# Kernel optimization log

Hardware: AMD Instinct MI355X
Metric: run time of the kernel (lower is better)

The kernel has to match this reference:

```python
import jax, jax.numpy as jnp
import numpy as np

N, D = 1024, 256  # number of matrices (power of 2), matrix dim
EPS = 0.002       # near-identity noise scale to keep 1024-long product stable


def setup_inputs() -> dict:
    key = jax.random.key(0)
    k1, k2 = jax.random.split(key)
    x = jax.random.normal(k1, (1, D), dtype=jnp.float32)
    m = jnp.eye(D, dtype=jnp.float32)[None] + EPS * jax.random.normal(
        k2, (N, D, D), dtype=jnp.float32)
    return {"x": x, "m": m}


def reference(x, m):
    # The torch module performs a Blelloch up-sweep (pairwise bmm) building
    # per-level products, then a down-sweep producing the exclusive prefix
    # applications of x: res[k] = x @ (m_0 @ ... @ m_{k-1}) for k = 0..N.
    # lax.associative_scan with matmul is the idiomatic log-depth tree scan
    # computing the same math: P[k] = m_0 @ ... @ m_k (inclusive, in order).
    P = jax.lax.associative_scan(jnp.matmul, m)      # [N, D, D]
    applied = jnp.matmul(x, P)[:, 0, :]              # [N, D]: x @ P[k]
    # res[0] = x (empty prefix), res[1..N] = x @ P[0..N-1]
    res = jnp.concatenate([x, applied], axis=0)      # [N+1, D]
    return res
```

## Files before the change

kernel.cpp:

```cpp
#include <hip/hip_runtime.h>
#include <hip/hip_bf16.h>


#define D 256
#define DD 65536

typedef __attribute__((ext_vector_type(8))) short short8;
typedef __attribute__((ext_vector_type(4))) float f4;

__device__ __forceinline__ float bf2f(unsigned short u) {
  return __uint_as_float(((unsigned)u) << 16);
}
__device__ __forceinline__ unsigned short f2bf(float f) {
  __hip_bfloat16 h = __float2bfloat16(f);
  unsigned short u;
  __builtin_memcpy(&u, &h, 2);
  return u;
}
__device__ __forceinline__ unsigned f2bf2(float lo, float hi) {
  __hip_bfloat162 h = __float22bfloat162_rn(make_float2(lo, hi));
  unsigned u;
  __builtin_memcpy(&u, &h, 4);
  return u;
}
#define LSWZ(i15, lq) (((((i15) & 15)) + ((lq) << 4)) ^ (lq))

__global__ __launch_bounds__(256, 4) void gemm_mfma(
    const float* __restrict__ aF, const unsigned short* __restrict__ aBf,
    long aMul, long aOff,
    const float* __restrict__ bF, const unsigned short* __restrict__ bBf,
    long bMul, long bOff,
    unsigned short* __restrict__ out)
{
  __shared__ __attribute__((aligned(16))) unsigned short Bs[16384];

  const int  bx  = blockIdx.x;
  const int  nmb = ((int)gridDim.x) >> 4;
  const int  xcd = bx & 7, q = bx >> 3;
  const long mat = (long)(xcd * (nmb >> 3)) + (q >> 4);
  const int  tile = q & 15;
  const int  m0 = (tile >> 2) << 6, n0 = (tile & 3) << 6;
  const long aBase = (mat * aMul + aOff) * (long)DD;
  const long bBase = (mat * bMul + bOff) * (long)DD;
  const int t = threadIdx.x;
  const int w = t >> 6, l = t & 63, lm = l & 15, lq4 = l >> 4;
  const int lswz = l ^ lq4;

  const int R = m0 + (w << 4) + lm;
  short8 areg[8];
  if (aF) {
    const float* ap = aF + aBase + (long)R * D + (lq4 << 3);
#pragma unroll
    for (int kt = 0; kt < 8; ++kt) {
      float4 v0 = *(const float4*)(ap + (kt << 5));
      float4 v1 = *(const float4*)(ap + (kt << 5) + 4);
      if ((R >> 3) == (kt << 2) + lq4) {
        const int j = R & 7;
        if      (j == 0) v0.x -= 1.f;
        else if (j == 1) v0.y -= 1.f;
        else if (j == 2) v0.z -= 1.f;
        else if (j == 3) v0.w -= 1.f;
        else if (j == 4) v1.x -= 1.f;
        else if (j == 5) v1.y -= 1.f;
        else if (j == 6) v1.z -= 1.f;
        else             v1.w -= 1.f;
      }
      union { short8 v8; unsigned u[4]; } ou;
      ou.u[0] = f2bf2(v0.x, v0.y);
      ou.u[1] = f2bf2(v0.z, v0.w);
      ou.u[2] = f2bf2(v1.x, v1.y);
      ou.u[3] = f2bf2(v1.z, v1.w);
      areg[kt] = ou.v8;
    }
  } else {
    const unsigned short* ap = aBf + aBase + (long)R * D + (lq4 << 3);
#pragma unroll
    for (int kt = 0; kt < 8; ++kt)
      areg[kt] = *(const short8*)(ap + (kt << 5));
  }

  {
    const int n4 = (t & 15) << 2;
    const int kb0 = (t >> 4) << 3;
    const int gn = n0 + n4;
#pragma unroll
    for (int kp = 0; kp < 2; ++kp) {
      const int k8 = kb0 + (kp << 7);
      const int lq = (k8 >> 3) & 3, kt = k8 >> 5;
      if (bF) {
        unsigned tmpu[4][4];
        const int rel = gn - k8;
#pragma unroll
        for (int h = 0; h < 2; ++h) {
          float4 va[2], vb[2];
#pragma unroll
          for (int p2 = 0; p2 < 2; ++p2) {
            va[p2] = *(const float4*)(bF + bBase + (long)(k8 + 4 * h + 2 * p2) * D + gn);
            vb[p2] = *(const float4*)(bF + bBase + (long)(k8 + 4 * h + 2 * p2 + 1) * D + gn);
          }
          if (rel == 4 * h) {
            va[0].x -= 1.f; vb[0].y -= 1.f; va[1].z -= 1.f; vb[1].w -= 1.f;
          }
          tmpu[0][2 * h + 0] = f2bf2(va[0].x, vb[0].x);
          tmpu[0][2 * h + 1] = f2bf2(va[1].x, vb[1].x);
          tmpu[1][2 * h + 0] = f2bf2(va[0].y, vb[0].y);
          tmpu[1][2 * h + 1] = f2bf2(va[1].y, vb[1].y);
          tmpu[2][2 * h + 0] = f2bf2(va[0].z, vb[0].z);
          tmpu[2][2 * h + 1] = f2bf2(va[1].z, vb[1].z);
          tmpu[3][2 * h + 0] = f2bf2(va[0].w, vb[0].w);
          tmpu[3][2 * h + 1] = f2bf2(va[1].w, vb[1].w);
        }
#pragma unroll
        for (int jj = 0; jj < 4; ++jj) {
          const int n = n4 + jj;
          const int slot = (((n >> 4) << 3) + kt) * 64 + LSWZ(n, lq);
          uint4 st = { tmpu[jj][0], tmpu[jj][1], tmpu[jj][2], tmpu[jj][3] };
          *(uint4*)&Bs[slot << 3] = st;
        }
      } else {
        __attribute__((aligned(16))) unsigned short tmp[4][8];
#pragma unroll
        for (int kk = 0; kk < 8; ++kk) {
          const ushort4 v = *(const ushort4*)(bBf + bBase + (long)(k8 + kk) * D + gn);
          tmp[0][kk] = v.x; tmp[1][kk] = v.y; tmp[2][kk] = v.z; tmp[3][kk] = v.w;
        }
#pragma unroll
        for (int jj = 0; jj < 4; ++jj) {
          const int n = n4 + jj;
          const int slot = (((n >> 4) << 3) + kt) * 64 + LSWZ(n, lq);
          *(uint4*)&Bs[slot << 3] = *(const uint4*)&tmp[jj][0];
        }
      }
    }
  }
  __syncthreads();

  f4 acc[4] = {{0.f,0.f,0.f,0.f},{0.f,0.f,0.f,0.f},
               {0.f,0.f,0.f,0.f},{0.f,0.f,0.f,0.f}};
#pragma unroll
  for (int kt = 0; kt < 8; ++kt) {
#pragma unroll
    for (int f = 0; f < 4; ++f) {
      const short8 b = *(const short8*)&Bs[((((f << 3) + kt) << 6) + lswz) << 3];
      acc[f] = __builtin_amdgcn_mfma_f32_16x16x32_bf16(areg[kt], b, acc[f], 0, 0, 0);
    }
  }

#pragma unroll
  for (int f = 0; f < 4; ++f) {
    const int gj_l = (f << 4) + lm;
    const int gj   = n0 + gj_l;
#pragma unroll
    for (int r = 0; r < 4; ++r) {
      const int gi_l = (w << 4) + (lq4 << 2) + r;
      const int giG  = m0 + gi_l;
      float da;
      if (aF)
        da = aF[aBase + (long)giG * D + gj] - ((giG == gj) ? 1.f : 0.f);
      else
        da = bf2f(aBf[aBase + (long)giG * D + gj]);
      const int lqB  = (giG >> 3) & 3;
      const int slotB = (((gj_l >> 4) << 3) + (giG >> 5)) * 64 + LSWZ(gj_l, lqB);
      const float db = bf2f(Bs[(slotB << 3) + (giG & 7)]);
      acc[f][r] += da + db;
    }
  }
  __syncthreads();

  unsigned short* Cs = Bs;
#pragma unroll
  for (int f = 0; f < 4; ++f)
#pragma unroll
    for (int r = 0; r < 4; ++r)
      Cs[((w << 4) + (lq4 << 2) + r) * 66 + (f << 4) + lm] = f2bf(acc[f][r]);
  __syncthreads();
  {
    const int row = t >> 2, c0g = (t & 3) << 4;
    const unsigned int* Cw = (const unsigned int*)Cs;
    const int wb = row * 33 + ((t & 3) << 3);
    unsigned int wbuf[8];
#pragma unroll
    for (int i = 0; i < 8; ++i) wbuf[i] = Cw[wb + i];
    unsigned short* og = out + mat * (long)DD + (long)(m0 + row) * D + n0 + c0g;
    uint4 o0 = { wbuf[0], wbuf[1], wbuf[2], wbuf[3] };
    uint4 o1 = { wbuf[4], wbuf[5], wbuf[6], wbuf[7] };
    *(uint4*)og = o0;
    *((uint4*)og + 1) = o1;
  }
}

__device__ __forceinline__ void apply_bf16(const unsigned short* __restrict__ Mb,
                                           float* v, float (*ps)[D],
                                           int t, int col4, int q) {
  const unsigned short* Mp = Mb + (long)(q * 16) * D + col4;
  float a0 = 0.f, a1 = 0.f, a2 = 0.f, a3 = 0.f;
#pragma unroll
  for (int i = 0; i < 16; ++i) {
    const ushort4 u = *(const ushort4*)(Mp + (long)i * D);
    const float vi = v[q * 16 + i];
    a0 += vi * bf2f(u.x); a1 += vi * bf2f(u.y);
    a2 += vi * bf2f(u.z); a3 += vi * bf2f(u.w);
  }
  *(float4*)&ps[q][col4] = make_float4(a0, a1, a2, a3);
  __syncthreads();
  if (t < D) {
    float s = 0.f;
#pragma unroll
    for (int j = 0; j < 16; ++j) s += ps[j][t];
    v[t] += s;
  }
  __syncthreads();
}

__global__ __launch_bounds__(1024) void tail_fused(
    const float* __restrict__ x,
    const unsigned short* __restrict__ sp128, const unsigned short* __restrict__ sp64,
    const unsigned short* __restrict__ sp32,  const unsigned short* __restrict__ sp16,
    const unsigned short* __restrict__ sp8,   const unsigned short* __restrict__ sp4,
    const float* __restrict__ m, float* __restrict__ out)
{
  __shared__ float v[D];
  __shared__ float ps[16][D];
  const int c = blockIdx.x, t = threadIdx.x;
  const int col4 = (t & 63) << 2, q = t >> 6;
  if (t < D) v[t] = x[t];
  __syncthreads();
  const int L = c << 2;

  int pos = 0;
#pragma unroll 1
  while (pos + 128 <= L) { apply_bf16(sp128 + (long)(pos >> 7) * DD, v, ps, t, col4, q); pos += 128; }
  if (pos + 64 <= L) { apply_bf16(sp64 + (long)(pos >> 6) * DD, v, ps, t, col4, q); pos += 64; }
  if (pos + 32 <= L) { apply_bf16(sp32 + (long)(pos >> 5) * DD, v, ps, t, col4, q); pos += 32; }
  if (pos + 16 <= L) { apply_bf16(sp16 + (long)(pos >> 4) * DD, v, ps, t, col4, q); pos += 16; }
  if (pos + 8 <= L)  { apply_bf16(sp8  + (long)(pos >> 3) * DD, v, ps, t, col4, q); pos += 8; }
  if (pos + 4 <= L)  { apply_bf16(sp4  + (long)(pos >> 2) * DD, v, ps, t, col4, q); pos += 4; }

  if (t < D) out[(long)L * D + t] = v[t];
  const int steps = (c == 255) ? 4 : 3;
#pragma unroll 1
  for (int s = 0; s < steps; ++s) {
    const float* Mp = m + (long)(L + s) * DD + (long)(q * 16) * D + col4;
    float a0 = 0.f, a1 = 0.f, a2 = 0.f, a3 = 0.f;
#pragma unroll
    for (int i = 0; i < 16; ++i) {
      const float4 u = *(const float4*)(Mp + (long)i * D);
      const float vi = v[q * 16 + i];
      a0 += vi * u.x; a1 += vi * u.y; a2 += vi * u.z; a3 += vi * u.w;
    }
    *(float4*)&ps[q][col4] = make_float4(a0, a1, a2, a3);
    __syncthreads();
    if (t < D) {
      float s2 = 0.f;
#pragma unroll
      for (int j = 0; j < 16; ++j) s2 += ps[j][t];
      v[t] = s2;
      out[(long)(L + s + 1) * D + t] = s2;
    }
    __syncthreads();
  }
}

__global__ __launch_bounds__(256) void fallback_seq(
    const float* __restrict__ x, const float* __restrict__ m,
    float* __restrict__ out)
{
  __shared__ float v[D];
  const int t = threadIdx.x;
  v[t] = x[t];
  __syncthreads();
  for (int k = 0; k < 1024; ++k) {
    out[(long)k * D + t] = v[t];
    const float* M = m + (long)k * DD;
    float acc = 0.f;
    for (int i = 0; i < D; ++i) acc += v[i] * M[(long)i * D + t];
    __syncthreads();
    v[t] = acc;
    __syncthreads();
  }
  out[(long)1024 * D + t] = v[t];
}

extern "C" void kernel_launch(void* const* d_in, const int* in_sizes, int n_in,
                              void* d_out, int out_size, void* d_ws, size_t ws_size,
                              hipStream_t stream) {
  const float* x = (const float*)d_in[0];
  const float* m = (const float*)d_in[1];
  float* out = (float*)d_out;

  char* w8 = (char*)d_ws;
  const size_t MB = 1048576;
  const dim3 blk(256), vblk(1024);

  if (ws_size >= 127 * MB) {
    unsigned short* T2   = (unsigned short*)(w8);
    unsigned short* Qb   = (unsigned short*)(w8 + 64 * MB);
    unsigned short* Q2   = (unsigned short*)(w8 + 96 * MB);
    unsigned short* Q4   = (unsigned short*)(w8 + 112 * MB);
    unsigned short* Rm   = (unsigned short*)(w8 + 120 * MB);
    unsigned short* S64  = (unsigned short*)(w8 + 124 * MB);
    unsigned short* S128 = (unsigned short*)(w8 + 126 * MB);
    gemm_mfma<<<dim3(8192), blk, 0, stream>>>(m, nullptr, 2, 0, m, nullptr, 2, 1, T2);
    gemm_mfma<<<dim3(4096), blk, 0, stream>>>(nullptr, T2, 2, 0, nullptr, T2, 2, 1, Qb);
    gemm_mfma<<<dim3(2048), blk, 0, stream>>>(nullptr, Qb, 2, 0, nullptr, Qb, 2, 1, Q2);
    gemm_mfma<<<dim3(1024), blk, 0, stream>>>(nullptr, Q2, 2, 0, nullptr, Q2, 2, 1, Q4);
    gemm_mfma<<<dim3(512),  blk, 0, stream>>>(nullptr, Q4, 2, 0, nullptr, Q4, 2, 1, Rm);
    gemm_mfma<<<dim3(256),  blk, 0, stream>>>(nullptr, Rm, 2, 0, nullptr, Rm, 2, 1, S64);
    gemm_mfma<<<dim3(128),  blk, 0, stream>>>(nullptr, S64, 2, 0, nullptr, S64, 2, 1, S128);
    tail_fused<<<dim3(256), vblk, 0, stream>>>(x, S128, S64, Rm, Q4, Q2, Qb, m, out);
  } else if (ws_size >= 67108864) {
    unsigned short* buf0 = (unsigned short*)(w8);
    unsigned short* Qb   = (unsigned short*)(w8 + 33554432);
    unsigned short* Q2   = (unsigned short*)(w8);
    unsigned short* Q4   = (unsigned short*)(w8 + 16777216);
    unsigned short* Rm   = (unsigned short*)(w8 + 25165824);
    unsigned short* S64  = (unsigned short*)(w8 + 29360128);
    unsigned short* S128 = (unsigned short*)(w8 + 31457280);
    gemm_mfma<<<dim3(4096), blk, 0, stream>>>(m, nullptr, 2, 0, m, nullptr, 2, 1, buf0);
    gemm_mfma<<<dim3(2048), blk, 0, stream>>>(nullptr, buf0, 2, 0, nullptr, buf0, 2, 1, Qb);
    gemm_mfma<<<dim3(4096), blk, 0, stream>>>(m + 512L * DD, nullptr, 2, 0,
                                              m + 512L * DD, nullptr, 2, 1, buf0);
    gemm_mfma<<<dim3(2048), blk, 0, stream>>>(nullptr, buf0, 2, 0, nullptr, buf0, 2, 1,
                                              Qb + 128L * DD);
    gemm_mfma<<<dim3(2048), blk, 0, stream>>>(nullptr, Qb, 2, 0, nullptr, Qb, 2, 1, Q2);
    gemm_mfma<<<dim3(1024), blk, 0, stream>>>(nullptr, Q2, 2, 0, nullptr, Q2, 2, 1, Q4);
    gemm_mfma<<<dim3(512),  blk, 0, stream>>>(nullptr, Q4, 2, 0, nullptr, Q4, 2, 1, Rm);
    gemm_mfma<<<dim3(256),  blk, 0, stream>>>(nullptr, Rm, 2, 0, nullptr, Rm, 2, 1, S64);
    gemm_mfma<<<dim3(128),  blk, 0, stream>>>(nullptr, S64, 2, 0, nullptr, S64, 2, 1, S128);
    tail_fused<<<dim3(256), vblk, 0, stream>>>(x, S128, S64, Rm, Q4, Q2, Qb, m, out);
  } else {
    fallback_seq<<<dim3(1), blk, 0, stream>>>(x, m, out);
  }
}
```

Before: 565.5 us.

## Store odd-indexed products transposed so later GEMMs read B directly without LDS staging

Each GEMM level now writes odd-indexed output matrices transposed. A new gemm_bt kernel can then load the B operand row-contiguously from global memory straight into MFMA registers, with no LDS staging of B. The tail kernel gets a transposed matrix-vector path for odd partial products. This removes the LDS transpose/staging cost in the upper levels, but B fragments are now read from global/L2 per wave with no shared reuse, and the transposed writes add LDS bank conflicts.

```diff
diff --git a/kernel.cpp b/kernel.cpp
--- a/kernel.cpp
+++ b/kernel.cpp
@@ -30,7 +30,7 @@
     long aMul, long aOff,
     const float* __restrict__ bF, const unsigned short* __restrict__ bBf,
     long bMul, long bOff,
-    unsigned short* __restrict__ out)
+    unsigned short* __restrict__ out, int wTodd)
 {
   __shared__ __attribute__((aligned(16))) unsigned short Bs[16384];
 
@@ -167,12 +167,15 @@
   }
   __syncthreads();
 
+  const int wT = wTodd & (int)(mat & 1);
   unsigned short* Cs = Bs;
 #pragma unroll
   for (int f = 0; f < 4; ++f)
 #pragma unroll
-    for (int r = 0; r < 4; ++r)
-      Cs[((w << 4) + (lq4 << 2) + r) * 66 + (f << 4) + lm] = f2bf(acc[f][r]);
+    for (int r = 0; r < 4; ++r) {
+      const int row_ = (w << 4) + (lq4 << 2) + r, col_ = (f << 4) + lm;
+      Cs[wT ? (col_ * 66 + row_) : (row_ * 66 + col_)] = f2bf(acc[f][r]);
+    }
   __syncthreads();
   {
     const int row = t >> 2, c0g = (t & 3) << 4;
@@ -181,7 +184,81 @@
     unsigned int wbuf[8];
 #pragma unroll
     for (int i = 0; i < 8; ++i) wbuf[i] = Cw[wb + i];
-    unsigned short* og = out + mat * (long)DD + (long)(m0 + row) * D + n0 + c0g;
+    unsigned short* og = out + mat * (long)DD +
+        (wT ? ((long)(n0 + row) * D + m0 + c0g)
+            : ((long)(m0 + row) * D + n0 + c0g));
+    uint4 o0 = { wbuf[0], wbuf[1], wbuf[2], wbuf[3] };
+    uint4 o1 = { wbuf[4], wbuf[5], wbuf[6], wbuf[7] };
+    *(uint4*)og = o0;
+    *((uint4*)og + 1) = o1;
+  }
+}
+
+__global__ __launch_bounds__(256, 4) void gemm_bt(
+    const unsigned short* __restrict__ in, unsigned short* __restrict__ out,
+    int wTodd)
+{
+  __shared__ __attribute__((aligned(16))) unsigned short Cs[4224];
+
+  const int  bx  = blockIdx.x;
+  const int  nmb = ((int)gridDim.x) >> 4;
+  const int  xcd = bx & 7, q = bx >> 3;
+  const long mat = (long)(xcd * (nmb >> 3)) + (q >> 4);
+  const int  tile = q & 15;
+  const int  m0 = (tile >> 2) << 6, n0 = (tile & 3) << 6;
+  const unsigned short* aBf = in + 2 * mat * (long)DD;
+  const unsigned short* bt  = in + (2 * mat + 1) * (long)DD;
+  const int t = threadIdx.x;
+  const int w = t >> 6, l = t & 63, lm = l & 15, lq4 = l >> 4;
+
+  const int R = m0 + (w << 4) + lm;
+  short8 areg[8];
+  const unsigned short* ap = aBf + (long)R * D + (lq4 << 3);
+#pragma unroll
+  for (int kt = 0; kt < 8; ++kt)
+    areg[kt] = *(const short8*)(ap + (kt << 5));
+
+  f4 acc[4] = {{0.f,0.f,0.f,0.f},{0.f,0.f,0.f,0.f},
+               {0.f,0.f,0.f,0.f},{0.f,0.f,0.f,0.f}};
+  const unsigned short* bp = bt + (long)(n0 + lm) * D + (lq4 << 3);
+#pragma unroll
+  for (int kt = 0; kt < 8; ++kt) {
+#pragma unroll
+    for (int f = 0; f < 4; ++f) {
+      const short8 b = *(const short8*)(bp + ((long)(f << 4)) * D + (kt << 5));
+      acc[f] = __builtin_amdgcn_mfma_f32_16x16x32_bf16(areg[kt], b, acc[f], 0, 0, 0);
+    }
+  }
+
+#pragma unroll
+  for (int f = 0; f < 4; ++f) {
+    const int gj = n0 + (f << 4) + lm;
+#pragma unroll
+    for (int r = 0; r < 4; ++r) {
+      const int giG = m0 + (w << 4) + (lq4 << 2) + r;
+      acc[f][r] += bf2f(aBf[(long)giG * D + gj]) + bf2f(bt[(long)gj * D + giG]);
+    }
+  }
+
+  const int wT = wTodd & (int)(mat & 1);
+#pragma unroll
+  for (int f = 0; f < 4; ++f)
+#pragma unroll
+    for (int r = 0; r < 4; ++r) {
+      const int row_ = (w << 4) + (lq4 << 2) + r, col_ = (f << 4) + lm;
+      Cs[wT ? (col_ * 66 + row_) : (row_ * 66 + col_)] = f2bf(acc[f][r]);
+    }
+  __syncthreads();
+  {
+    const int row = t >> 2, c0g = (t & 3) << 4;
+    const unsigned int* Cw = (const unsigned int*)Cs;
+    const int wb = row * 33 + ((t & 3) << 3);
+    unsigned int wbuf[8];
+#pragma unroll
+    for (int i = 0; i < 8; ++i) wbuf[i] = Cw[wb + i];
+    unsigned short* og = out + mat * (long)DD +
+        (wT ? ((long)(n0 + row) * D + m0 + c0g)
+            : ((long)(m0 + row) * D + n0 + c0g));
     uint4 o0 = { wbuf[0], wbuf[1], wbuf[2], wbuf[3] };
     uint4 o1 = { wbuf[4], wbuf[5], wbuf[6], wbuf[7] };
     *(uint4*)og = o0;
@@ -212,12 +289,41 @@
   __syncthreads();
 }
 
+__device__ __forceinline__ void apply_bf16_t(const unsigned short* __restrict__ Mt,
+                                             float* v, float (*ps)[D],
+                                             int t, int col4, int q) {
+  float a[4];
+#pragma unroll
+  for (int j = 0; j < 4; ++j) {
+    const unsigned short* p = Mt + (long)(col4 + j) * D + q * 16;
+    const short8 u0 = *(const short8*)p;
+    const short8 u1 = *(const short8*)(p + 8);
+    float s = 0.f;
+#pragma unroll
+    for (int i = 0; i < 8; ++i)
+      s += v[q * 16 + i] * bf2f((unsigned short)u0[i]);
+#pragma unroll
+    for (int i = 0; i < 8; ++i)
+      s += v[q * 16 + 8 + i] * bf2f((unsigned short)u1[i]);
+    a[j] = s;
+  }
+  *(float4*)&ps[q][col4] = make_float4(a[0], a[1], a[2], a[3]);
+  __syncthreads();
+  if (t < D) {
+    float s = 0.f;
+#pragma unroll
+    for (int j = 0; j < 16; ++j) s += ps[j][t];
+    v[t] += s;
+  }
+  __syncthreads();
+}
+
 __global__ __launch_bounds__(1024) void tail_fused(
     const float* __restrict__ x,
     const unsigned short* __restrict__ sp128, const unsigned short* __restrict__ sp64,
     const unsigned short* __restrict__ sp32,  const unsigned short* __restrict__ sp16,
     const unsigned short* __restrict__ sp8,   const unsigned short* __restrict__ sp4,
-    const float* __restrict__ m, float* __restrict__ out)
+    const float* __restrict__ m, float* __restrict__ out, int trOdd)
 {
   __shared__ float v[D];
   __shared__ float ps[16][D];
@@ -227,14 +333,25 @@
   __syncthreads();
   const int L = c << 2;
 
+#define APPLY_P(base, idx)                                              \
+  do {                                                                  \
+    if (trOdd && (((idx) & 1) != 0))                                    \
+      apply_bf16_t((base) + (long)(idx) * DD, v, ps, t, col4, q);       \
+    else                                                                \
+      apply_bf16((base) + (long)(idx) * DD, v, ps, t, col4, q);         \
+  } while (0)
+
   int pos = 0;
 #pragma unroll 1
-  while (pos + 128 <= L) { apply_bf16(sp128 + (long)(pos >> 7) * DD, v, ps, t, col4, q); pos += 128; }
-  if (pos + 64 <= L) { apply_bf16(sp64 + (long)(pos >> 6) * DD, v, ps, t, col4, q); pos += 64; }
-  if (pos + 32 <= L) { apply_bf16(sp32 + (long)(pos >> 5) * DD, v, ps, t, col4, q); pos += 32; }
-  if (pos + 16 <= L) { apply_bf16(sp16 + (long)(pos >> 4) * DD, v, ps, t, col4, q); pos += 16; }
-  if (pos + 8 <= L)  { apply_bf16(sp8  + (long)(pos >> 3) * DD, v, ps, t, col4, q); pos += 8; }
-  if (pos + 4 <= L)  { apply_bf16(sp4  + (long)(pos >> 2) * DD, v, ps, t, col4, q); pos += 4; }
+  while (pos + 128 <= L) {
+    apply_bf16(sp128 + (long)(pos >> 7) * DD, v, ps, t, col4, q); pos += 128;
+  }
+  if (pos + 64 <= L) { APPLY_P(sp64, pos >> 6); pos += 64; }
+  if (pos + 32 <= L) { APPLY_P(sp32, pos >> 5); pos += 32; }
+  if (pos + 16 <= L) { APPLY_P(sp16, pos >> 4); pos += 16; }
+  if (pos + 8 <= L)  { APPLY_P(sp8,  pos >> 3); pos += 8; }
+  if (pos + 4 <= L)  { APPLY_P(sp4,  pos >> 2); pos += 4; }
+#undef APPLY_P
 
   if (t < D) out[(long)L * D + t] = v[t];
   const int steps = (c == 255) ? 4 : 3;
@@ -300,14 +417,14 @@
     unsigned short* Rm   = (unsigned short*)(w8 + 120 * MB);
     unsigned short* S64  = (unsigned short*)(w8 + 124 * MB);
     unsigned short* S128 = (unsigned short*)(w8 + 126 * MB);
-    gemm_mfma<<<dim3(8192), blk, 0, stream>>>(m, nullptr, 2, 0, m, nullptr, 2, 1, T2);
-    gemm_mfma<<<dim3(4096), blk, 0, stream>>>(nullptr, T2, 2, 0, nullptr, T2, 2, 1, Qb);
-    gemm_mfma<<<dim3(2048), blk, 0, stream>>>(nullptr, Qb, 2, 0, nullptr, Qb, 2, 1, Q2);
-    gemm_mfma<<<dim3(1024), blk, 0, stream>>>(nullptr, Q2, 2, 0, nullptr, Q2, 2, 1, Q4);
-    gemm_mfma<<<dim3(512),  blk, 0, stream>>>(nullptr, Q4, 2, 0, nullptr, Q4, 2, 1, Rm);
-    gemm_mfma<<<dim3(256),  blk, 0, stream>>>(nullptr, Rm, 2, 0, nullptr, Rm, 2, 1, S64);
-    gemm_mfma<<<dim3(128),  blk, 0, stream>>>(nullptr, S64, 2, 0, nullptr, S64, 2, 1, S128);
-    tail_fused<<<dim3(256), vblk, 0, stream>>>(x, S128, S64, Rm, Q4, Q2, Qb, m, out);
+    gemm_mfma<<<dim3(8192), blk, 0, stream>>>(m, nullptr, 2, 0, m, nullptr, 2, 1, T2, 1);
+    gemm_bt<<<dim3(4096), blk, 0, stream>>>(T2,  Qb,   1);
+    gemm_bt<<<dim3(2048), blk, 0, stream>>>(Qb,  Q2,   1);
+    gemm_bt<<<dim3(1024), blk, 0, stream>>>(Q2,  Q4,   1);
+    gemm_bt<<<dim3(512),  blk, 0, stream>>>(Q4,  Rm,   1);
+    gemm_bt<<<dim3(256),  blk, 0, stream>>>(Rm,  S64,  1);
+    gemm_bt<<<dim3(128),  blk, 0, stream>>>(S64, S128, 0);
+    tail_fused<<<dim3(256), vblk, 0, stream>>>(x, S128, S64, Rm, Q4, Q2, Qb, m, out, 1);
   } else if (ws_size >= 67108864) {
     unsigned short* buf0 = (unsigned short*)(w8);
     unsigned short* Qb   = (unsigned short*)(w8 + 33554432);
@@ -316,18 +433,18 @@
     unsigned short* Rm   = (unsigned short*)(w8 + 25165824);
     unsigned short* S64  = (unsigned short*)(w8 + 29360128);
     unsigned short* S128 = (unsigned short*)(w8 + 31457280);
-    gemm_mfma<<<dim3(4096), blk, 0, stream>>>(m, nullptr, 2, 0, m, nullptr, 2, 1, buf0);
-    gemm_mfma<<<dim3(2048), blk, 0, stream>>>(nullptr, buf0, 2, 0, nullptr, buf0, 2, 1, Qb);
+    gemm_mfma<<<dim3(4096), blk, 0, stream>>>(m, nullptr, 2, 0, m, nullptr, 2, 1, buf0, 0);
+    gemm_mfma<<<dim3(2048), blk, 0, stream>>>(nullptr, buf0, 2, 0, nullptr, buf0, 2, 1, Qb, 0);
     gemm_mfma<<<dim3(4096), blk, 0, stream>>>(m + 512L * DD, nullptr, 2, 0,
-                                              m + 512L * DD, nullptr, 2, 1, buf0);
+                                              m + 512L * DD, nullptr, 2, 1, buf0, 0);
     gemm_mfma<<<dim3(2048), blk, 0, stream>>>(nullptr, buf0, 2, 0, nullptr, buf0, 2, 1,
-                                              Qb + 128L * DD);
-    gemm_mfma<<<dim3(2048), blk, 0, stream>>>(nullptr, Qb, 2, 0, nullptr, Qb, 2, 1, Q2);
-    gemm_mfma<<<dim3(1024), blk, 0, stream>>>(nullptr, Q2, 2, 0, nullptr, Q2, 2, 1, Q4);
-    gemm_mfma<<<dim3(512),  blk, 0, stream>>>(nullptr, Q4, 2, 0, nullptr, Q4, 2, 1, Rm);
-    gemm_mfma<<<dim3(256),  blk, 0, stream>>>(nullptr, Rm, 2, 0, nullptr, Rm, 2, 1, S64);
-    gemm_mfma<<<dim3(128),  blk, 0, stream>>>(nullptr, S64, 2, 0, nullptr, S64, 2, 1, S128);
-    tail_fused<<<dim3(256), vblk, 0, stream>>>(x, S128, S64, Rm, Q4, Q2, Qb, m, out);
+                                              Qb + 128L * DD, 0);
+    gemm_mfma<<<dim3(2048), blk, 0, stream>>>(nullptr, Qb, 2, 0, nullptr, Qb, 2, 1, Q2, 0);
+    gemm_mfma<<<dim3(1024), blk, 0, stream>>>(nullptr, Q2, 2, 0, nullptr, Q2, 2, 1, Q4, 0);
+    gemm_mfma<<<dim3(512),  blk, 0, stream>>>(nullptr, Q4, 2, 0, nullptr, Q4, 2, 1, Rm, 0);
+    gemm_mfma<<<dim3(256),  blk, 0, stream>>>(nullptr, Rm, 2, 0, nullptr, Rm, 2, 1, S64, 0);
+    gemm_mfma<<<dim3(128),  blk, 0, stream>>>(nullptr, S64, 2, 0, nullptr, S64, 2, 1, S128, 0);
+    tail_fused<<<dim3(256), vblk, 0, stream>>>(x, S128, S64, Rm, Q4, Q2, Qb, m, out, 0);
   } else {
     fallback_seq<<<dim3(1), blk, 0, stream>>>(x, m, out);
   }
```

Result: slower. 650.1 us (+15.0%).
